# Optimization experiments

Hardware: AMD Instinct MI355X
Metric: run time of the kernel (lower is better)

Reference implementation:

```python
import jax, jax.numpy as jnp
import numpy as np

B, S, H, L, NH, FF, V, NL = 16, 512, 768, 12, 12, 3072, 30522, 9
DH = H // NH


def setup_inputs() -> dict:
    key = jax.random.key(0)
    ks = iter(jax.random.split(key, 16))
    def w(shape, scale=0.02):
        return jax.random.normal(next(ks), shape, jnp.float32) * scale
    return {
        "input_word_ids": jax.random.randint(next(ks), (B, S), 0, V, jnp.int32),
        "input_mask": jnp.ones((B, S), jnp.int32),
        "input_type_ids": jnp.zeros((B, S), jnp.int32),
        "valid_mask": jax.random.randint(next(ks), (B, S), 0, 2, jnp.int32),
        "word_emb": w((V, H)),
        "pos_emb": w((S, H)),
        "type_emb": w((2, H)),
        "emb_ln_g": jnp.ones((H,), jnp.float32),
        "emb_ln_b": jnp.zeros((H,), jnp.float32),
        "Wq": w((L, H, H)), "bq": jnp.zeros((L, H), jnp.float32),
        "Wk": w((L, H, H)), "bk": jnp.zeros((L, H), jnp.float32),
        "Wv": w((L, H, H)), "bv": jnp.zeros((L, H), jnp.float32),
        "Wo": w((L, H, H)), "bo": jnp.zeros((L, H), jnp.float32),
        "ln1_g": jnp.ones((L, H), jnp.float32), "ln1_b": jnp.zeros((L, H), jnp.float32),
        "W1": w((L, H, FF)), "b1": jnp.zeros((L, FF), jnp.float32),
        "W2": w((L, FF, H)), "b2": jnp.zeros((L, H), jnp.float32),
        "ln2_g": jnp.ones((L, H), jnp.float32), "ln2_b": jnp.zeros((L, H), jnp.float32),
        "cls_W": w((H, NL)), "cls_b": jnp.zeros((NL,), jnp.float32),
    }


def _layer_norm(x, g, b):
    m = x.mean(-1, keepdims=True)
    v = ((x - m) ** 2).mean(-1, keepdims=True)
    return (x - m) * jax.lax.rsqrt(v + 1e-12) * g + b


def reference(input_word_ids, input_mask, input_type_ids, valid_mask,
              word_emb, pos_emb, type_emb, emb_ln_g, emb_ln_b,
              Wq, bq, Wk, bk, Wv, bv, Wo, bo, ln1_g, ln1_b,
              W1, b1, W2, b2, ln2_g, ln2_b, cls_W, cls_b):
    b, s = input_word_ids.shape
    # --- BERT embeddings ---
    x = word_emb[input_word_ids] + pos_emb[None, :s] + type_emb[input_type_ids]
    x = _layer_norm(x, emb_ln_g, emb_ln_b)  # [B,S,H]
    attn_bias = (1.0 - input_mask.astype(jnp.float32))[:, None, None, :] * -1e9
    scale = 1.0 / np.sqrt(DH).astype(np.float32)

    def step(h, p):
        wq, bq_, wk, bk_, wv, bv_, wo, bo_, g1, gb1, w1, wb1, w2, wb2, g2, gb2 = p
        q = (h @ wq + bq_).reshape(b, s, NH, DH)
        k = (h @ wk + bk_).reshape(b, s, NH, DH)
        v = (h @ wv + bv_).reshape(b, s, NH, DH)
        scores = jnp.einsum('bqhd,bkhd->bhqk', q, k) * scale + attn_bias
        probs = jax.nn.softmax(scores, axis=-1)
        ctx = jnp.einsum('bhqk,bkhd->bqhd', probs, v).reshape(b, s, H)
        h = _layer_norm(h + ctx @ wo + bo_, g1, gb1)
        ff = jax.nn.gelu(h @ w1 + wb1, approximate=False)
        h = _layer_norm(h + ff @ w2 + wb2, g2, gb2)
        return h, None

    params = (Wq, bq, Wk, bk, Wv, bv, Wo, bo, ln1_g, ln1_b, W1, b1, W2, b2, ln2_g, ln2_b)
    x, _ = jax.lax.scan(step, x, params)

    # --- valid-token compaction (vectorized form of the python double loop) ---
    # valid tokens packed to the front (stable order), remainder zero-padded
    invalid = (1 - valid_mask).astype(jnp.int32)
    perm = jnp.argsort(invalid, axis=1, stable=True)          # [B,S]
    compact = jnp.take_along_axis(x, perm[:, :, None], axis=1)
    counts = valid_mask.sum(axis=1)                           # [B]
    keep = (jnp.arange(s)[None, :] < counts[:, None])[:, :, None]
    compact = jnp.where(keep, compact, jnp.zeros((), x.dtype))
    # dropout is identity at inference (training=False)
    logits = jax.nn.softmax(compact @ cls_W + cls_b, axis=-1)  # [B,S,NL]
    return logits
```

## Files before the change

### kernel.cpp

```cpp
#include <hip/hip_runtime.h>
#include <cstdint>
#include <cstddef>

#define B_ 16
#define S_ 512
#define H_ 768
#define L_ 12
#define NH_ 12
#define DH_ 64
#define FF_ 3072
#define NL_ 9
#define QKV_ 2304

typedef _Float16 f16x8 __attribute__((ext_vector_type(8)));
typedef float f32x4 __attribute__((ext_vector_type(4)));

__device__ __forceinline__ void load_lds16(const void* g, void* l) {
  __builtin_amdgcn_global_load_lds(
      (const __attribute__((address_space(1))) unsigned int*)g,
      (__attribute__((address_space(3))) unsigned int*)l, 16, 0, 0);
}

__device__ __forceinline__ float block_sum256(float v, float* red) {
#pragma unroll
  for (int off = 32; off; off >>= 1) v += __shfl_down(v, off);
  __syncthreads();
  if ((threadIdx.x & 63) == 0) red[threadIdx.x >> 6] = v;
  __syncthreads();
  return red[0] + red[1] + red[2] + red[3];
}

__device__ __forceinline__ float gelu_f(float x) {
  return 0.5f * x * (1.0f + erff(x * 0.70710678118654752f));
}

__global__ __launch_bounds__(256) void embed_ln_kernel(
    const int* __restrict__ wid, const int* __restrict__ tpid,
    const float* __restrict__ we, const float* __restrict__ pe,
    const float* __restrict__ te, const float* __restrict__ g,
    const float* __restrict__ bb, float* __restrict__ h,
    _Float16* __restrict__ hb) {
  __shared__ float red[4];
  int tok = blockIdx.x;
  int s = tok & (S_ - 1);
  int w = wid[tok], tp = tpid[tok];
  int t = threadIdx.x;
  float x[3];
#pragma unroll
  for (int i = 0; i < 3; ++i) {
    int j = t + i * 256;
    x[i] = we[(size_t)w * H_ + j] + pe[(size_t)s * H_ + j] + te[(size_t)tp * H_ + j];
  }
  float m = block_sum256(x[0] + x[1] + x[2], red) * (1.0f / H_);
  float d0 = x[0] - m, d1 = x[1] - m, d2 = x[2] - m;
  float var = block_sum256(d0 * d0 + d1 * d1 + d2 * d2, red) * (1.0f / H_);
  float rs = rsqrtf(var + 1e-12f);
#pragma unroll
  for (int i = 0; i < 3; ++i) {
    int j = t + i * 256;
    float v = (x[i] - m) * rs * g[j] + bb[j];
    h[(size_t)tok * H_ + j] = v;
    hb[(size_t)tok * H_ + j] = (_Float16)v;
  }
}

__global__ __launch_bounds__(256) void add_ln_kernel(
    float* __restrict__ h, const float* __restrict__ delta,
    const float* __restrict__ g, const float* __restrict__ bb,
    _Float16* __restrict__ hb) {
  __shared__ float red[4];
  int tok = blockIdx.x;
  int t = threadIdx.x;
  float x[3];
#pragma unroll
  for (int i = 0; i < 3; ++i) {
    int j = t + i * 256;
    x[i] = h[(size_t)tok * H_ + j] + delta[(size_t)tok * H_ + j];
  }
  float m = block_sum256(x[0] + x[1] + x[2], red) * (1.0f / H_);
  float d0 = x[0] - m, d1 = x[1] - m, d2 = x[2] - m;
  float var = block_sum256(d0 * d0 + d1 * d1 + d2 * d2, red) * (1.0f / H_);
  float rs = rsqrtf(var + 1e-12f);
#pragma unroll
  for (int i = 0; i < 3; ++i) {
    int j = t + i * 256;
    float v = (x[i] - m) * rs * g[j] + bb[j];
    h[(size_t)tok * H_ + j] = v;
    hb[(size_t)tok * H_ + j] = (_Float16)v;
  }
}

__global__ __launch_bounds__(256) void convert_weights_kernel(
    const float* __restrict__ Wq, const float* __restrict__ Wk,
    const float* __restrict__ Wv, const float* __restrict__ Wo,
    const float* __restrict__ W1, const float* __restrict__ W2,
    _Float16* __restrict__ qT, _Float16* __restrict__ kT,
    _Float16* __restrict__ vT, _Float16* __restrict__ oT,
    _Float16* __restrict__ w1T, _Float16* __restrict__ w2T,
    const float* __restrict__ bq, const float* __restrict__ bk,
    const float* __restrict__ bv, float* __restrict__ qkvb) {
  int id = blockIdx.x;
  int tid = threadIdx.x;
  if (id == 1728) {
    for (int j = tid; j < H_; j += 256) {
      qkvb[j] = bq[j];
      qkvb[H_ + j] = bk[j];
      qkvb[2 * H_ + j] = bv[j];
    }
    return;
  }
  __shared__ float T[64][65];
  const float* src;
  _Float16* dst;
  int K, N, tk, tn;
  if (id < 576) {
    int mat = id / 144, t = id % 144;
    K = 768; N = 768; tk = t / 12; tn = t % 12;
    src = (mat == 0) ? Wq : (mat == 1) ? Wk : (mat == 2) ? Wv : Wo;
    dst = (mat == 0) ? qT : (mat == 1) ? kT : (mat == 2) ? vT : oT;
  } else if (id < 1152) {
    int t = id - 576; K = 768; N = 3072; tk = t / 48; tn = t % 48;
    src = W1; dst = w1T;
  } else {
    int t = id - 1152; K = 3072; N = 768; tk = t / 12; tn = t % 12;
    src = W2; dst = w2T;
  }
  int k0 = tk * 64, n0 = tn * 64;
  {
    int r = tid >> 4, c4 = (tid & 15) * 4;
#pragma unroll
    for (int i = 0; i < 4; ++i) {
      float4 v = *(const float4*)&src[(size_t)(k0 + r + i * 16) * N + n0 + c4];
      T[r + i * 16][c4 + 0] = v.x;
      T[r + i * 16][c4 + 1] = v.y;
      T[r + i * 16][c4 + 2] = v.z;
      T[r + i * 16][c4 + 3] = v.w;
    }
  }
  __syncthreads();
#pragma unroll
  for (int i = 0; i < 2; ++i) {
    int chunk = tid + i * 256;
    int n = chunk >> 3, kc = (chunk & 7) * 8;
    f16x8 o;
#pragma unroll
    for (int j = 0; j < 8; ++j) o[j] = (_Float16)T[kc + j][n];
    *(f16x8*)&dst[(size_t)(n0 + n) * K + k0 + kc] = o;
  }
}

template <int OUT>
__global__ __launch_bounds__(256) void gemm_f16(
    const _Float16* __restrict__ A, const _Float16* __restrict__ Bt,
    const float* __restrict__ bias, void* __restrict__ Cv,
    int M, int N, int K) {
  __shared__ _Float16 As[3][128 * 32];
  __shared__ _Float16 Bs[3][128 * 32];
  int tid = threadIdx.x;
  int lane = tid & 63, w = tid >> 6;
  int wr = w >> 1, wc = w & 1;
  int l15 = lane & 15, kb = lane >> 4;
  int swk = (l15 >> 1) & 3;

  int nwg = gridDim.x * gridDim.y;
  int bid = blockIdx.y * gridDim.x + blockIdx.x;
  int swz = bid;
  if ((nwg & 7) == 0) {
    int cpx = nwg >> 3;
    swz = (bid & 7) * cpx + (bid >> 3);
  }
  int bx = swz % gridDim.x, by = swz / gridDim.x;
  int row0 = by * 128, col0 = bx * 128;

  int srow = lane >> 2;
  int schunk = (lane & 3) ^ ((lane >> 3) & 3);
  int scol = schunk * 8;
  const _Float16* gA0 = A + (size_t)(row0 + (w * 2 + 0) * 16 + srow) * K + scol;
  const _Float16* gA1 = A + (size_t)(row0 + (w * 2 + 1) * 16 + srow) * K + scol;
  const _Float16* gB0 = Bt + (size_t)(col0 + (w * 2 + 0) * 16 + srow) * K + scol;
  const _Float16* gB1 = Bt + (size_t)(col0 + (w * 2 + 1) * 16 + srow) * K + scol;
  int o0 = (w * 2 + 0) * 1024;
  int o1 = (w * 2 + 1) * 1024;

  auto STAGE = [&](int t, int buf) {
    int ko = t * 32;
    load_lds16(gA0 + ko, (char*)&As[buf][0] + o0);
    load_lds16(gA1 + ko, (char*)&As[buf][0] + o1);
    load_lds16(gB0 + ko, (char*)&Bs[buf][0] + o0);
    load_lds16(gB1 + ko, (char*)&Bs[buf][0] + o1);
  };

  f32x4 acc[4][4] = {};
  int nk = K >> 5;

  STAGE(0, 0);
  STAGE(1, 1);
  asm volatile("s_waitcnt vmcnt(4)" ::: "memory");
  __builtin_amdgcn_s_barrier();
  __builtin_amdgcn_sched_barrier(0);

  for (int t = 0; t < nk; ++t) {
    int buf = t % 3;
    if (t + 2 < nk) {
      STAGE(t + 2, (t + 2) % 3);
      asm volatile("s_waitcnt vmcnt(8)" ::: "memory");
    } else if (t + 1 < nk) {
      asm volatile("s_waitcnt vmcnt(4)" ::: "memory");
    } else {
      asm volatile("s_waitcnt vmcnt(0)" ::: "memory");
    }
    __builtin_amdgcn_s_barrier();
    __builtin_amdgcn_sched_barrier(0);
    f16x8 af[4], bf[4];
    int rpos = (kb ^ swk) * 8;
#pragma unroll
    for (int m = 0; m < 4; ++m)
      af[m] = *(const f16x8*)&As[buf][(wr * 64 + m * 16 + l15) * 32 + rpos];
#pragma unroll
    for (int n = 0; n < 4; ++n)
      bf[n] = *(const f16x8*)&Bs[buf][(wc * 64 + n * 16 + l15) * 32 + rpos];
#pragma unroll
    for (int m = 0; m < 4; ++m)
#pragma unroll
      for (int n = 0; n < 4; ++n)
        acc[m][n] = __builtin_amdgcn_mfma_f32_16x16x32_f16(af[m], bf[n], acc[m][n], 0, 0, 0);
    asm volatile("s_waitcnt lgkmcnt(0)" ::: "memory");
    __builtin_amdgcn_sched_barrier(0);
    __builtin_amdgcn_s_barrier();
  }
#pragma unroll
  for (int n = 0; n < 4; ++n) {
    int col = col0 + wc * 64 + n * 16 + l15;
    float bv = bias[col];
#pragma unroll
    for (int m = 0; m < 4; ++m) {
      int rowb = row0 + wr * 64 + m * 16 + kb * 4;
#pragma unroll
      for (int r = 0; r < 4; ++r) {
        float v = acc[m][n][r] + bv;
        if (OUT == 2) v = gelu_f(v);
        if (OUT == 0)
          ((float*)Cv)[(size_t)(rowb + r) * N + col] = v;
        else
          ((_Float16*)Cv)[(size_t)(rowb + r) * N + col] = (_Float16)v;
      }
    }
  }
}

__global__ __launch_bounds__(256) void vtrans_kernel(
    const _Float16* __restrict__ v, int RS, _Float16* __restrict__ vt) {
  __shared__ _Float16 T[64][72];
  int s0 = blockIdx.x * 64;
  int bh = blockIdx.y;
  int b = bh / NH_, h = bh % NH_;
  int tid = threadIdx.x;
#pragma unroll
  for (int i = 0; i < 2; ++i) {
    int chunk = tid + i * 256;
    int s = chunk >> 3, dc = (chunk & 7) * 8;
    *(f16x8*)&T[s][dc] = *(const f16x8*)&v[(size_t)(b * S_ + s0 + s) * RS + h * DH_ + dc];
  }
  __syncthreads();
#pragma unroll
  for (int i = 0; i < 2; ++i) {
    int chunk = tid + i * 256;
    int d = chunk >> 3, sc = (chunk & 7) * 8;
    f16x8 o;
#pragma unroll
    for (int j = 0; j < 8; ++j) o[j] = T[sc + j][d];
    *(f16x8*)&vt[(size_t)(bh * DH_ + d) * S_ + s0 + sc] = o;
  }
}

__global__ __launch_bounds__(256) void flash_attn_kernel(
    const _Float16* __restrict__ q, const _Float16* __restrict__ k,
    const _Float16* __restrict__ vt, int RS, const int* __restrict__ mask,
    _Float16* __restrict__ ctx) {
  __shared__ _Float16 Ks[128 * 72];
  __shared__ _Float16 Vs[64 * 136];
  __shared__ _Float16 Ps[4][16 * 136];
  __shared__ float biasz[S_];
  int qt = blockIdx.x, h = blockIdx.y, b = blockIdx.z;
  int tid = threadIdx.x, lane = tid & 63, w = tid >> 6;
  int l15 = lane & 15, kb = lane >> 4;
  const float C = 0.125f * 1.44269504088896f;

  for (int i = tid; i < S_; i += 256)
    biasz[i] = (1.0f - (float)mask[b * S_ + i]) * (-1e9f * C);

  int qrow = b * S_ + qt * 64 + w * 16 + l15;
  f16x8 qf[2];
  qf[0] = *(const f16x8*)&q[(size_t)qrow * RS + h * DH_ + kb * 8];
  qf[1] = *(const f16x8*)&q[(size_t)qrow * RS + h * DH_ + 32 + kb * 8];

  auto loadKV = [&](int kt, f16x8* rk, f16x8* rv) {
#pragma unroll
    for (int i = 0; i < 4; ++i) {
      int idx = tid + i * 256;
      int r = idx >> 3, c = idx & 7;
      rk[i] = *(const f16x8*)&k[(size_t)(b * S_ + kt * 128 + r) * RS + h * DH_ + c * 8];
      int d = idx >> 4, c2 = idx & 15;
      rv[i] = *(const f16x8*)&vt[(size_t)((b * NH_ + h) * DH_ + d) * S_ + kt * 128 + c2 * 8];
    }
  };

  float m_run[4], l_run[4];
  f32x4 o[4] = {};
#pragma unroll
  for (int r = 0; r < 4; ++r) { m_run[r] = -1e30f; l_run[r] = 0.f; }

  f16x8 rk[4], rv[4];
  loadKV(0, rk, rv);
  for (int kt = 0; kt < 4; ++kt) {
    __syncthreads();
#pragma unroll
    for (int i = 0; i < 4; ++i) {
      int idx = tid + i * 256;
      int r = idx >> 3, c = idx & 7;
      *(f16x8*)&Ks[r * 72 + c * 8] = rk[i];
      int d = idx >> 4, c2 = idx & 15;
      *(f16x8*)&Vs[d * 136 + c2 * 8] = rv[i];
    }
    __syncthreads();
    if (kt < 3) loadKV(kt + 1, rk, rv);
    f32x4 s[8];
#pragma unroll
    for (int nf = 0; nf < 8; ++nf) {
      f16x8 b0 = *(const f16x8*)&Ks[(nf * 16 + l15) * 72 + kb * 8];
      f16x8 b1 = *(const f16x8*)&Ks[(nf * 16 + l15) * 72 + 32 + kb * 8];
      f32x4 z = {};
      z = __builtin_amdgcn_mfma_f32_16x16x32_f16(qf[0], b0, z, 0, 0, 0);
      z = __builtin_amdgcn_mfma_f32_16x16x32_f16(qf[1], b1, z, 0, 0, 0);
      s[nf] = z;
    }
    float zb[8];
#pragma unroll
    for (int nf = 0; nf < 8; ++nf) zb[nf] = biasz[kt * 128 + nf * 16 + l15];
    float pw[8][4];
    float corr[4];
#pragma unroll
    for (int r = 0; r < 4; ++r) {
      float mx = -1e30f;
#pragma unroll
      for (int nf = 0; nf < 8; ++nf) mx = fmaxf(mx, s[nf][r] * C + zb[nf]);
#pragma unroll
      for (int d = 1; d < 16; d <<= 1) mx = fmaxf(mx, __shfl_xor(mx, d));
      float mnew = fmaxf(m_run[r], mx);
      float cr = exp2f(m_run[r] - mnew);
      m_run[r] = mnew;
      corr[r] = cr;
      float sum = 0.f;
#pragma unroll
      for (int nf = 0; nf < 8; ++nf) {
        float pv = exp2f(s[nf][r] * C + zb[nf] - mnew);
        pw[nf][r] = pv;
        sum += pv;
      }
#pragma unroll
      for (int d = 1; d < 16; d <<= 1) sum += __shfl_xor(sum, d);
      l_run[r] = l_run[r] * cr + sum;
    }
#pragma unroll
    for (int nf2 = 0; nf2 < 4; ++nf2)
#pragma unroll
      for (int r = 0; r < 4; ++r) o[nf2][r] *= corr[r];
#pragma unroll
    for (int nf = 0; nf < 8; ++nf)
#pragma unroll
      for (int r = 0; r < 4; ++r)
        Ps[w][(kb * 4 + r) * 136 + nf * 16 + l15] = (_Float16)pw[nf][r];
#pragma unroll
    for (int ks = 0; ks < 4; ++ks) {
      f16x8 pa = *(const f16x8*)&Ps[w][l15 * 136 + ks * 32 + kb * 8];
#pragma unroll
      for (int nf2 = 0; nf2 < 4; ++nf2) {
        f16x8 vb2 = *(const f16x8*)&Vs[(nf2 * 16 + l15) * 136 + ks * 32 + kb * 8];
        o[nf2] = __builtin_amdgcn_mfma_f32_16x16x32_f16(pa, vb2, o[nf2], 0, 0, 0);
      }
    }
  }
  float inv[4];
#pragma unroll
  for (int r = 0; r < 4; ++r) inv[r] = 1.0f / fmaxf(l_run[r], 1e-37f);
#pragma unroll
  for (int nf2 = 0; nf2 < 4; ++nf2)
#pragma unroll
    for (int r = 0; r < 4; ++r) {
      int row = b * S_ + qt * 64 + w * 16 + kb * 4 + r;
      ctx[(size_t)row * H_ + h * DH_ + nf2 * 16 + l15] = (_Float16)(o[nf2][r] * inv[r]);
    }
}

__global__ void compact_idx_kernel(const int* __restrict__ valid, int* __restrict__ dest) {
  int b = threadIdx.x;
  if (b >= B_) return;
  int cnt = 0;
  for (int s = 0; s < S_; ++s) {
    int vv = valid[b * S_ + s];
    dest[b * S_ + s] = vv ? cnt : -1;
    cnt += vv;
  }
}

__global__ __launch_bounds__(256) void scatter_kernel(
    const float* __restrict__ h, const int* __restrict__ dest,
    float* __restrict__ compact) {
  int tok = blockIdx.x;
  int d = dest[tok];
  if (d < 0) return;
  int b = tok >> 9;
  size_t src = (size_t)tok * H_;
  size_t dst = ((size_t)(b * S_ + d)) * H_;
  for (int j = threadIdx.x; j < H_; j += 256) compact[dst + j] = h[src + j];
}

__global__ __launch_bounds__(256) void cls_kernel(
    const float* __restrict__ x, const float* __restrict__ W,
    const float* __restrict__ bias2, float* __restrict__ out) {
  int lane = threadIdx.x & 63, wv = threadIdx.x >> 6;
  int tok = blockIdx.x * 4 + wv;
  float acc[NL_] = {};
  for (int hh = lane; hh < H_; hh += 64) {
    float xv = x[(size_t)tok * H_ + hh];
#pragma unroll
    for (int n = 0; n < NL_; ++n) acc[n] = fmaf(xv, W[hh * NL_ + n], acc[n]);
  }
#pragma unroll
  for (int n = 0; n < NL_; ++n) {
#pragma unroll
    for (int off = 32; off; off >>= 1) acc[n] += __shfl_down(acc[n], off);
  }
  if (lane == 0) {
    float vls[NL_], mx = -1e30f;
#pragma unroll
    for (int n = 0; n < NL_; ++n) {
      vls[n] = acc[n] + bias2[n];
      mx = fmaxf(mx, vls[n]);
    }
    float s = 0.f;
#pragma unroll
    for (int n = 0; n < NL_; ++n) {
      vls[n] = expf(vls[n] - mx);
      s += vls[n];
    }
    float inv = 1.0f / s;
#pragma unroll
    for (int n = 0; n < NL_; ++n) out[(size_t)tok * NL_ + n] = vls[n] * inv;
  }
}

extern "C" void kernel_launch(void* const* d_in, const int* in_sizes, int n_in,
                              void* d_out, int out_size, void* d_ws, size_t ws_size,
                              hipStream_t stream) {
  const int* wid = (const int*)d_in[0];
  const int* mask = (const int*)d_in[1];
  const int* tpid = (const int*)d_in[2];
  const int* valid = (const int*)d_in[3];
  const float* we = (const float*)d_in[4];
  const float* pe = (const float*)d_in[5];
  const float* te = (const float*)d_in[6];
  const float* eg = (const float*)d_in[7];
  const float* eb = (const float*)d_in[8];
  const float* Wq = (const float*)d_in[9];
  const float* bq = (const float*)d_in[10];
  const float* Wk = (const float*)d_in[11];
  const float* bk = (const float*)d_in[12];
  const float* Wv = (const float*)d_in[13];
  const float* bv = (const float*)d_in[14];
  const float* Wo = (const float*)d_in[15];
  const float* bo = (const float*)d_in[16];
  const float* g1 = (const float*)d_in[17];
  const float* gb1 = (const float*)d_in[18];
  const float* W1 = (const float*)d_in[19];
  const float* bf1 = (const float*)d_in[20];
  const float* W2 = (const float*)d_in[21];
  const float* bf2 = (const float*)d_in[22];
  const float* g2 = (const float*)d_in[23];
  const float* gb2 = (const float*)d_in[24];
  const float* cW = (const float*)d_in[25];
  const float* cb = (const float*)d_in[26];
  float* out = (float*)d_out;

  const size_t TOK = (size_t)B_ * S_;
  char* ws = (char*)d_ws;
  float* h = (float*)ws;
  _Float16* hb = (_Float16*)(ws + 25165824);
  float* t1 = (float*)(ws + 37748736);
  char* un1 = ws + 62914560;
  _Float16* qkv = (_Float16*)un1;
  _Float16* vt = (_Float16*)(un1 + 37748736);
  _Float16* ffh = (_Float16*)un1;
  _Float16* ctx = (_Float16*)(ws + 113246208);
  char* wbuf = ws + 125829120;
  _Float16* wqT = (_Float16*)wbuf;
  _Float16* wkT = (_Float16*)(wbuf + 1179648);
  _Float16* wvT = (_Float16*)(wbuf + 2359296);
  _Float16* woT = (_Float16*)(wbuf + 3538944);
  _Float16* w1T = (_Float16*)(wbuf + 4718592);
  _Float16* w2T = (_Float16*)(wbuf + 9437184);
  int* dest = (int*)(ws + 139984896);
  float* qkvb = (float*)(ws + 140017664);

  dim3 blk(256);
  embed_ln_kernel<<<dim3((unsigned)TOK), blk, 0, stream>>>(wid, tpid, we, pe, te, eg, eb, h, hb);

  dim3 gQKV(QKV_ / 128, TOK / 128);
  dim3 gH(H_ / 128, TOK / 128);
  dim3 gF(FF_ / 128, TOK / 128);
  for (int l = 0; l < L_; ++l) {
    convert_weights_kernel<<<dim3(1729), blk, 0, stream>>>(
        Wq + (size_t)l * H_ * H_, Wk + (size_t)l * H_ * H_,
        Wv + (size_t)l * H_ * H_, Wo + (size_t)l * H_ * H_,
        W1 + (size_t)l * H_ * FF_, W2 + (size_t)l * FF_ * H_,
        wqT, wkT, wvT, woT, w1T, w2T,
        bq + l * H_, bk + l * H_, bv + l * H_, qkvb);
    gemm_f16<1><<<gQKV, blk, 0, stream>>>(hb, wqT, qkvb, qkv, (int)TOK, QKV_, H_);
    vtrans_kernel<<<dim3(S_ / 64, B_ * NH_), blk, 0, stream>>>(qkv + 2 * H_, QKV_, vt);
    flash_attn_kernel<<<dim3(S_ / 64, NH_, B_), blk, 0, stream>>>(
        qkv, qkv + H_, vt, QKV_, mask, ctx);
    gemm_f16<0><<<gH, blk, 0, stream>>>(ctx, woT, bo + l * H_, t1, (int)TOK, H_, H_);
    add_ln_kernel<<<dim3((unsigned)TOK), blk, 0, stream>>>(h, t1, g1 + l * H_, gb1 + l * H_, hb);
    gemm_f16<2><<<gF, blk, 0, stream>>>(hb, w1T, bf1 + l * FF_, ffh, (int)TOK, FF_, H_);
    gemm_f16<0><<<gH, blk, 0, stream>>>(ffh, w2T, bf2 + l * H_, t1, (int)TOK, H_, FF_);
    add_ln_kernel<<<dim3((unsigned)TOK), blk, 0, stream>>>(h, t1, g2 + l * H_, gb2 + l * H_, hb);
  }

  compact_idx_kernel<<<1, 64, 0, stream>>>(valid, dest);
  hipMemsetAsync(t1, 0, TOK * H_ * sizeof(float), stream);
  scatter_kernel<<<dim3((unsigned)TOK), blk, 0, stream>>>(h, dest, t1);
  cls_kernel<<<dim3((unsigned)(TOK / 4)), blk, 0, stream>>>(t1, cW, cb, out);
}
```

Measured before the change: 3.693 ms.

## Add 128x256-tile GEMM for QKV and FFN1, use polynomial erf in GELU

Adds a new GEMM kernel with 128x256 output tiles and double-buffered LDS, where each wave owns a 128x64 sub-tile, and uses it for the QKV and FFN-up projections. The larger tile raises arithmetic intensity per LDS load and halves the number of workgroups for these wide-N GEMMs. GELU now uses the Abramowitz-Stegun polynomial approximation of erf with a fast exp instead of erff, which cuts the cost of the FFN1 epilogue but introduces a small approximation error (about 1e-7 absolute in erf). The 128 accumulator registers per thread create register pressure that may limit occupancy despite the launch bound of two blocks.

Result: slower. 3.860 ms (+4.5%).

```diff
diff --git a/kernel.cpp b/kernel.cpp
--- a/kernel.cpp
+++ b/kernel.cpp
@@ -31,7 +31,13 @@
 }
 
 __device__ __forceinline__ float gelu_f(float x) {
-  return 0.5f * x * (1.0f + erff(x * 0.70710678118654752f));
+  float au = fabsf(x) * 0.70710678118654752f;
+  float t = 1.0f / (1.0f + 0.3275911f * au);
+  float p = ((((1.061405429f * t - 1.453152027f) * t + 1.421413741f) * t
+              - 0.284496736f) * t + 0.254829592f) * t;
+  float e = p * __expf(-au * au);
+  float phi = (x >= 0.0f) ? (1.0f - 0.5f * e) : (0.5f * e);
+  return x * phi;
 }
 
 __global__ __launch_bounds__(256) void embed_ln_kernel(
@@ -146,6 +152,98 @@
 #pragma unroll
     for (int j = 0; j < 8; ++j) o[j] = (_Float16)T[kc + j][n];
     *(f16x8*)&dst[(size_t)(n0 + n) * K + k0 + kc] = o;
+  }
+}
+
+template <int OUT>
+__global__ __launch_bounds__(256, 2) void gemm_f16w(
+    const _Float16* __restrict__ A, const _Float16* __restrict__ Bt,
+    const float* __restrict__ bias, void* __restrict__ Cv,
+    int M, int N, int K) {
+  __shared__ _Float16 As[2][128 * 32];
+  __shared__ _Float16 Bs[2][256 * 32];
+  int tid = threadIdx.x;
+  int lane = tid & 63, w = tid >> 6;
+  int l15 = lane & 15, kb = lane >> 4;
+  int swk = (l15 >> 1) & 3;
+
+  int nwg = gridDim.x * gridDim.y;
+  int bid = blockIdx.y * gridDim.x + blockIdx.x;
+  int swz = bid;
+  if ((nwg & 7) == 0) {
+    int cpx = nwg >> 3;
+    swz = (bid & 7) * cpx + (bid >> 3);
+  }
+  int bx = swz % gridDim.x, by = swz / gridDim.x;
+  int row0 = by * 128, col0 = bx * 256;
+
+  int srow = lane >> 2;
+  int schunk = (lane & 3) ^ ((lane >> 3) & 3);
+  int scol = schunk * 8;
+  const _Float16* gA0 = A + (size_t)(row0 + (w * 2 + 0) * 16 + srow) * K + scol;
+  const _Float16* gA1 = A + (size_t)(row0 + (w * 2 + 1) * 16 + srow) * K + scol;
+  const _Float16* gB0 = Bt + (size_t)(col0 + (w * 4 + 0) * 16 + srow) * K + scol;
+  const _Float16* gB1 = Bt + (size_t)(col0 + (w * 4 + 1) * 16 + srow) * K + scol;
+  const _Float16* gB2 = Bt + (size_t)(col0 + (w * 4 + 2) * 16 + srow) * K + scol;
+  const _Float16* gB3 = Bt + (size_t)(col0 + (w * 4 + 3) * 16 + srow) * K + scol;
+  int oA0 = (w * 2 + 0) * 1024, oA1 = (w * 2 + 1) * 1024;
+  int oB0 = (w * 4 + 0) * 1024, oB1 = (w * 4 + 1) * 1024;
+  int oB2 = (w * 4 + 2) * 1024, oB3 = (w * 4 + 3) * 1024;
+
+  f32x4 acc[8][4] = {};
+  int nk = K >> 5;
+
+  load_lds16(gA0, (char*)&As[0][0] + oA0);
+  load_lds16(gA1, (char*)&As[0][0] + oA1);
+  load_lds16(gB0, (char*)&Bs[0][0] + oB0);
+  load_lds16(gB1, (char*)&Bs[0][0] + oB1);
+  load_lds16(gB2, (char*)&Bs[0][0] + oB2);
+  load_lds16(gB3, (char*)&Bs[0][0] + oB3);
+  __syncthreads();
+
+  for (int t = 0; t < nk; ++t) {
+    int cur = t & 1;
+    if (t + 1 < nk) {
+      int ko = (t + 1) * 32;
+      load_lds16(gA0 + ko, (char*)&As[cur ^ 1][0] + oA0);
+      load_lds16(gA1 + ko, (char*)&As[cur ^ 1][0] + oA1);
+      load_lds16(gB0 + ko, (char*)&Bs[cur ^ 1][0] + oB0);
+      load_lds16(gB1 + ko, (char*)&Bs[cur ^ 1][0] + oB1);
+      load_lds16(gB2 + ko, (char*)&Bs[cur ^ 1][0] + oB2);
+      load_lds16(gB3 + ko, (char*)&Bs[cur ^ 1][0] + oB3);
+    }
+    int rpos = (kb ^ swk) * 8;
+    f16x8 af[8], bf[4];
+#pragma unroll
+    for (int m = 0; m < 8; ++m)
+      af[m] = *(const f16x8*)&As[cur][(m * 16 + l15) * 32 + rpos];
+#pragma unroll
+    for (int n = 0; n < 4; ++n)
+      bf[n] = *(const f16x8*)&Bs[cur][(w * 64 + n * 16 + l15) * 32 + rpos];
+#pragma unroll
+    for (int m = 0; m < 8; ++m)
+#pragma unroll
+      for (int n = 0; n < 4; ++n)
+        acc[m][n] = __builtin_amdgcn_mfma_f32_16x16x32_f16(af[m], bf[n], acc[m][n], 0, 0, 0);
+    __syncthreads();
+  }
+#pragma unroll
+  for (int n = 0; n < 4; ++n) {
+    int col = col0 + w * 64 + n * 16 + l15;
+    float bv = bias[col];
+#pragma unroll
+    for (int m = 0; m < 8; ++m) {
+      int rowb = row0 + m * 16 + kb * 4;
+#pragma unroll
+      for (int r = 0; r < 4; ++r) {
+        float v = acc[m][n][r] + bv;
+        if (OUT == 2) v = gelu_f(v);
+        if (OUT == 0)
+          ((float*)Cv)[(size_t)(rowb + r) * N + col] = v;
+        else
+          ((_Float16*)Cv)[(size_t)(rowb + r) * N + col] = (_Float16)v;
+      }
+    }
   }
 }
 
@@ -505,9 +603,9 @@
   dim3 blk(256);
   embed_ln_kernel<<<dim3((unsigned)TOK), blk, 0, stream>>>(wid, tpid, we, pe, te, eg, eb, h, hb);
 
-  dim3 gQKV(QKV_ / 128, TOK / 128);
+  dim3 gQKVw(QKV_ / 256, TOK / 128);
+  dim3 gF1w(FF_ / 256, TOK / 128);
   dim3 gH(H_ / 128, TOK / 128);
-  dim3 gF(FF_ / 128, TOK / 128);
   for (int l = 0; l < L_; ++l) {
     convert_weights_kernel<<<dim3(1729), blk, 0, stream>>>(
         Wq + (size_t)l * H_ * H_, Wk + (size_t)l * H_ * H_,
@@ -515,13 +613,13 @@
         W1 + (size_t)l * H_ * FF_, W2 + (size_t)l * FF_ * H_,
         wqT, wkT, wvT, woT, w1T, w2T,
         bq + l * H_, bk + l * H_, bv + l * H_, qkvb);
-    gemm_f16<1><<<gQKV, blk, 0, stream>>>(hb, wqT, qkvb, qkv, (int)TOK, QKV_, H_);
+    gemm_f16w<1><<<gQKVw, blk, 0, stream>>>(hb, wqT, qkvb, qkv, (int)TOK, QKV_, H_);
     vtrans_kernel<<<dim3(S_ / 64, B_ * NH_), blk, 0, stream>>>(qkv + 2 * H_, QKV_, vt);
     flash_attn_kernel<<<dim3(S_ / 64, NH_, B_), blk, 0, stream>>>(
         qkv, qkv + H_, vt, QKV_, mask, ctx);
     gemm_f16<0><<<gH, blk, 0, stream>>>(ctx, woT, bo + l * H_, t1, (int)TOK, H_, H_);
     add_ln_kernel<<<dim3((unsigned)TOK), blk, 0, stream>>>(h, t1, g1 + l * H_, gb1 + l * H_, hb);
-    gemm_f16<2><<<gF, blk, 0, stream>>>(hb, w1T, bf1 + l * FF_, ffh, (int)TOK, FF_, H_);
+    gemm_f16w<2><<<gF1w, blk, 0, stream>>>(hb, w1T, bf1 + l * FF_, ffh, (int)TOK, FF_, H_);
     gemm_f16<0><<<gH, blk, 0, stream>>>(ffh, w2T, bf2 + l * H_, t1, (int)TOK, H_, FF_);
     add_ln_kernel<<<dim3((unsigned)TOK), blk, 0, stream>>>(h, t1, g2 + l * H_, gb2 + l * H_, hb);
   }
```
